# Kernel tuning notes

Hardware: AMD Instinct MI355X
Metric: run time of the kernel (lower is better)

Reference implementation:

```python
import jax, jax.numpy as jnp
from jax import lax
import numpy as np

SHAPE = (50, 60, 65)   # -> after net: (17, 27, 32), flatten = 14688
NEG = 0.01             # LeakyReLU default slope
B, N = 8, 80000        # batch size, total active voxels


def _lrelu(x):
    return jnp.where(x >= 0, x, NEG * x)


def _sparse_conv(x, w, b, m):
    # Regular (non-submanifold) sparse conv == dense VALID conv on densified
    # input (inactive sites are 0 so they contribute nothing). Output site is
    # active iff any input site in the kernel footprint is active; bias is
    # added only at active output sites.
    k = w.shape[2]
    y = lax.conv_general_dilated(x, w, (1, 1, 1), 'VALID',
                                 dimension_numbers=('NCDHW', 'OIDHW', 'NCDHW'))
    m2 = lax.reduce_window(m, 0.0, lax.max, (1, 1, k, k, k), (1, 1, 1, 1, 1), 'VALID')
    y = jnp.where(m2 > 0, y + b[None, :, None, None, None], 0.0)
    return y, m2


def _sparse_maxpool(x, m, k):
    # spconv SparseMaxPool: max over ACTIVE sites only (inactive excluded, not 0)
    xm = jnp.where(m > 0, x, -jnp.inf)
    p = lax.reduce_window(xm, -jnp.inf, lax.max, (1, 1, k, k, k), (1, 1, 1, 1, 1), 'VALID')
    m2 = lax.reduce_window(m, 0.0, lax.max, (1, 1, k, k, k), (1, 1, 1, 1, 1), 'VALID')
    return jnp.where(m2 > 0, p, 0.0), m2


def setup_inputs() -> dict:
    key = jax.random.key(0)
    ks = jax.random.split(key, 24)
    D, H, W = SHAPE
    features = jax.random.normal(ks[0], (N, 1), dtype=jnp.float32)
    bi = jax.random.randint(ks[1], (N,), 0, B)
    zi = jax.random.randint(ks[2], (N,), 0, D)
    yi = jax.random.randint(ks[3], (N,), 0, H)
    xi = jax.random.randint(ks[4], (N,), 0, W)
    coors = jnp.stack([bi, zi, yi, xi], axis=1).astype(jnp.int32)
    s = 0.05
    p = {}
    p['w1'] = jax.random.normal(ks[5], (32, 1, 4, 4, 4), jnp.float32) * s
    p['b1'] = jax.random.normal(ks[6], (32,), jnp.float32) * s
    p['w2'] = jax.random.normal(ks[7], (32, 32, 4, 4, 4), jnp.float32) * s
    p['b2'] = jax.random.normal(ks[8], (32,), jnp.float32) * s
    p['w3'] = jax.random.normal(ks[9], (32, 32, 4, 4, 4), jnp.float32) * s
    p['b3'] = jax.random.normal(ks[10], (32,), jnp.float32) * s
    p['w4'] = jax.random.normal(ks[11], (32, 32, 4, 4, 4), jnp.float32) * s
    p['b4'] = jax.random.normal(ks[12], (32,), jnp.float32) * s
    p['w5'] = jax.random.normal(ks[13], (32, 32, 4, 4, 4), jnp.float32) * s
    p['b5'] = jax.random.normal(ks[14], (32,), jnp.float32) * s
    p['w6'] = jax.random.normal(ks[15], (32, 32, 4, 4, 4), jnp.float32) * s
    p['b6'] = jax.random.normal(ks[16], (32,), jnp.float32) * s
    p['w7'] = jax.random.normal(ks[17], (1, 32, 4, 4, 4), jnp.float32) * s
    p['b7'] = jax.random.normal(ks[18], (1,), jnp.float32) * s
    p['W8'] = jax.random.normal(ks[19], (14688, 1000), jnp.float32) * 0.01
    p['b8'] = jax.random.normal(ks[20], (1000,), jnp.float32) * s
    p['W9'] = jax.random.normal(ks[21], (1000, 1000), jnp.float32) * 0.03
    p['b9'] = jax.random.normal(ks[22], (1000,), jnp.float32) * s
    p['W10'] = jax.random.normal(ks[23], (1000, 1), jnp.float32) * 0.03
    p['b10'] = jnp.zeros((1,), jnp.float32)
    return dict(features=features, coors=coors, batch_size=B, **p)


def reference(features, coors, batch_size,
              w1, b1, w2, b2, w3, b3, w4, b4, w5, b5, w6, b6, w7, b7,
              W8, b8, W9, b9, W10, b10):
    D, H, W = SHAPE
    bi, zi, yi, xi = coors[:, 0], coors[:, 1], coors[:, 2], coors[:, 3]
    dense = jnp.zeros((batch_size, 1, D, H, W), features.dtype)
    dense = dense.at[bi, 0, zi, yi, xi].set(features[:, 0])
    mask = jnp.zeros((batch_size, 1, D, H, W), features.dtype)
    mask = mask.at[bi, 0, zi, yi, xi].set(1.0)

    x, m = _sparse_conv(dense, w1, b1, mask); x = _lrelu(x)
    x, m = _sparse_conv(x, w2, b2, m);        x = _lrelu(x)
    x, m = _sparse_maxpool(x, m, 5)
    x, m = _sparse_conv(x, w3, b3, m);        x = _lrelu(x)
    x, m = _sparse_conv(x, w4, b4, m);        x = _lrelu(x)
    x, m = _sparse_maxpool(x, m, 5)
    x, m = _sparse_conv(x, w5, b5, m);        x = _lrelu(x)
    x, m = _sparse_conv(x, w6, b6, m);        x = _lrelu(x)
    x, m = _sparse_conv(x, w7, b7, m);        x = _lrelu(x)
    x, m = _sparse_maxpool(x, m, 5)

    # ToDense (inactive sites already 0) + Flatten -> [B, 14688]
    h = x.reshape(x.shape[0], -1)
    h = _lrelu(h @ W8 + b8)
    h = _lrelu(h @ W9 + b9)
    out = _lrelu(h @ W10 + b10)
    return out
```

## Files before the change

### kernel.cpp

```cpp
#include <hip/hip_runtime.h>
#include <cstddef>


#define NEGSLOPE 0.01f
#define NINF (-3.0e38f)

#define TZ 4
#define TY 4
#define TXT 16
#define IZ 7
#define IY 7
#define IX 19
#define NV (IZ*IY*IX)

#define PCZ 10

typedef __attribute__((ext_vector_type(8)))  short    short8;
typedef __attribute__((ext_vector_type(4)))  unsigned uint4v;
typedef __attribute__((ext_vector_type(16))) float    floatx16;

constexpr int ilog2c(int v) { return v == 1 ? 0 : 1 + ilog2c(v / 2); }

__device__ __forceinline__ float lrelu(float v) { return v >= 0.f ? v : NEGSLOPE * v; }

__device__ __forceinline__ unsigned short f2bf(float f) {
  unsigned b = __float_as_uint(f);
  return (unsigned short)((b + 0x7fffu + ((b >> 16) & 1u)) >> 16);
}
__device__ __forceinline__ float bf2f(unsigned short h) {
  return __uint_as_float(((unsigned)h) << 16);
}
__device__ __forceinline__ unsigned splitpair(float a, float b, unsigned& lo) {
  unsigned short ha = f2bf(a), hb = f2bf(b);
  unsigned short la = f2bf(a - bf2f(ha)), lb = f2bf(b - bf2f(hb));
  lo = (unsigned)la | ((unsigned)lb << 16);
  return (unsigned)ha | ((unsigned)hb << 16);
}

__device__ __forceinline__ float4 max4(float4 a, float4 b) {
  float4 r;
  r.x = fmaxf(a.x, b.x); r.y = fmaxf(a.y, b.y);
  r.z = fmaxf(a.z, b.z); r.w = fmaxf(a.w, b.w);
  return r;
}

__device__ __forceinline__ short8 ld_frag(const uint2* s2, int v, int oct) {
  uint2 u0 = s2[v * 5 + oct * 2];
  uint2 u1 = s2[v * 5 + oct * 2 + 1];
  uint4v t; t.x = u0.x; t.y = u0.y; t.z = u1.x; t.w = u1.y;
  return __builtin_bit_cast(short8, t);
}

__global__ void k_claim(const int* __restrict__ coors, unsigned* __restrict__ claim, int N) {
  int i = blockIdx.x * blockDim.x + threadIdx.x;
  if (i >= N) return;
  int b = coors[4*i], z = coors[4*i+1], y = coors[4*i+2], x = coors[4*i+3];
  int v = ((b*50 + z)*60 + y)*65 + x;
  atomicMax(&claim[v], (unsigned)(i + 1));
}

__global__ void k_scatter(const int* __restrict__ coors, const float* __restrict__ feat,
                          const unsigned* __restrict__ claim,
                          float* __restrict__ x0, float* __restrict__ m0, int N) {
  int i = blockIdx.x * blockDim.x + threadIdx.x;
  if (i >= N) return;
  int b = coors[4*i], z = coors[4*i+1], y = coors[4*i+2], x = coors[4*i+3];
  int v = ((b*50 + z)*60 + y)*65 + x;
  m0[v] = 1.f;
  if (claim[v] == (unsigned)(i + 1)) x0[v] = feat[i];
}

__global__ void k_repack(const float* __restrict__ w, float* __restrict__ wr, int CI, int CO) {
  int i = blockIdx.x * blockDim.x + threadIdx.x;
  int tot = CO * CI * 64;
  if (i >= tot) return;
  int k = i & 63;
  int ci = (i >> 6) % CI;
  int co = i / (64 * CI);
  wr[(k * CI + ci) * CO + co] = w[i];
}

__global__ void k_repack_mfma5(const float* __restrict__ wA, const float* __restrict__ wB,
                               const float* __restrict__ wC, const float* __restrict__ wD,
                               const float* __restrict__ wE, unsigned short* __restrict__ tbl0) {
  int layer = blockIdx.y;
  const float* w = layer == 0 ? wA : layer == 1 ? wB : layer == 2 ? wC
                 : layer == 3 ? wD : wE;
  unsigned short* tbl = tbl0 + (size_t)layer * 262144;
  int i = blockIdx.x * blockDim.x + threadIdx.x;
  if (i >= 64*4*2*64) return;
  int lane = i & 63; int t = i >> 6;
  int pack = t & 1; t >>= 1;
  int pass = t & 3; int tap = t >> 2;
  int co = lane & 31; int oct = lane >> 5;
#pragma unroll
  for (int j = 0; j < 8; ++j) {
    int k = oct * 8 + j;
    int ci = pass * 8 + (k & 7);
    int part = ((k >> 3) ^ pack) & 1;
    float wv = w[((co * 32 + ci) << 6) + tap];
    unsigned short wh = f2bf(wv);
    unsigned short r = part ? f2bf(wv - bf2f(wh)) : wh;
    tbl[(size_t)i * 8 + j] = r;
  }
}

template<int K>
__global__ __launch_bounds__(256, 4)
void kd_fused(const float* __restrict__ in, float* __restrict__ out,
              int Zi, int Yi, int Xi, int Zo, int Yo, int Xo,
              int tilesZ, int tilesY, int tilesX) {
  constexpr int TDZ = 4, TDY = 8, TDX = 32;
  constexpr int HZ = TDZ + K - 1, HY = TDY + K - 1, HX = TDX + K - 1;
  __shared__ float sA[HZ * HY * HX];
  __shared__ float sB[TDZ * HY * HX];
  __shared__ float sC[TDZ * TDY * HX];
  int bid = blockIdx.x;
  int txi = bid % tilesX; bid /= tilesX;
  int tyi = bid % tilesY; bid /= tilesY;
  int tzi = bid % tilesZ; int item = bid / tilesZ;
  const int z0 = tzi * TDZ, y0 = tyi * TDY, x0 = txi * TDX;
  const int tid = threadIdx.x;
  const float* ib = in + (size_t)item * Zi * Yi * Xi;

  for (int idx = tid; idx < HZ * HY * HX; idx += 256) {
    int iz = idx / (HY * HX); int r = idx - iz * (HY * HX);
    int iy = r / HX; int ix = r - iy * HX;
    int gz = z0 + iz, gy = y0 + iy, gx = x0 + ix;
    float v = 0.f;
    if (gz < Zi && gy < Yi && gx < Xi) v = ib[((size_t)gz * Yi + gy) * Xi + gx];
    sA[idx] = v;
  }
  __syncthreads();
  for (int idx = tid; idx < TDZ * HY * HX; idx += 256) {
    int z = idx / (HY * HX); int r = idx - z * (HY * HX);
    float m = 0.f;
#pragma unroll
    for (int d = 0; d < K; ++d) m = fmaxf(m, sA[(z + d) * (HY * HX) + r]);
    sB[idx] = m;
  }
  __syncthreads();
  for (int idx = tid; idx < TDZ * TDY * HX; idx += 256) {
    int z = idx / (TDY * HX); int r = idx - z * (TDY * HX);
    int y = r / HX; int x = r - y * HX;
    float m = 0.f;
#pragma unroll
    for (int d = 0; d < K; ++d) m = fmaxf(m, sB[z * (HY * HX) + (y + d) * HX + x]);
    sC[idx] = m;
  }
  __syncthreads();
  const int perOut = Zo * Yo * Xo;
  for (int idx = tid; idx < TDZ * TDY * TDX; idx += 256) {
    int z = idx / (TDY * TDX); int r = idx - z * (TDY * TDX);
    int y = r / TDX; int x = r - y * TDX;
    int gz = z0 + z, gy = y0 + y, gx = x0 + x;
    if (gz < Zo && gy < Yo && gx < Xo) {
      float m = 0.f;
#pragma unroll
      for (int d = 0; d < K; ++d) m = fmaxf(m, sC[z * (TDY * HX) + y * HX + x + d]);
      out[(size_t)item * perOut + ((size_t)gz * Yo + gy) * Xo + gx] = m;
    }
  }
}

template<int TZL, int TYL, int TXL, int IZL, int IYL, int IXL, bool POOLOUT>
__global__ __launch_bounds__(256, 4)
void k_conv32m(const float* __restrict__ in, const unsigned short* __restrict__ tbl,
               const float* __restrict__ bias, const float* __restrict__ mo,
               float* __restrict__ out,
               int Zi, int Yi, int Xi, int Zo, int Yo, int Xo,
               int tilesZ, int tilesY, int tilesX) {
  constexpr int NVL = IZL * IYL * IXL;
  constexpr int LXs = ilog2c(TXL);
  constexpr int LYs = ilog2c(TYL);
  __shared__ unsigned sU[NVL * 10];
  const int perIn = Zi * Yi * Xi;
  const int perOut = Zo * Yo * Xo;
  int bid = blockIdx.x;
  int txi = bid % tilesX; bid /= tilesX;
  int tyi = bid % tilesY; bid /= tilesY;
  int tzi = bid % tilesZ; int item = bid / tilesZ;
  const int z0 = tzi * TZL, y0 = tyi * TYL, x0 = txi * TXL;
  const int tid = threadIdx.x;
  const int lane = tid & 63;
  const int col = lane & 31;
  const int oct = lane >> 5;
  const int wv  = tid >> 6;

  int lvBase0, lvBase1;
  {
    int vt0 = (2*wv + 0)*32 + col;
    int vt1 = (2*wv + 1)*32 + col;
    lvBase0 = ((vt0 >> (LXs+LYs))*IYL + ((vt0 >> LXs) & (TYL-1)))*IXL + (vt0 & (TXL-1));
    lvBase1 = ((vt1 >> (LXs+LYs))*IYL + ((vt1 >> LXs) & (TYL-1)))*IXL + (vt1 & (TXL-1));
  }

  floatx16 acc0, acc1;
#pragma unroll
  for (int r = 0; r < 16; ++r) { acc0[r] = 0.f; acc1[r] = 0.f; }

  const float* inb = in + (size_t)item * perIn * 32;
  const char* tb = (const char*)tbl + lane * 16;
  uint2* s2 = (uint2*)sU;

#pragma unroll 1
  for (int p = 0; p < 4; ++p) {
    __syncthreads();
    for (int idx = tid; idx < NVL; idx += 256) {
      int iz = idx / (IYL * IXL); int r = idx - iz * (IYL * IXL);
      int iy = r / IXL; int ix = r - iy * IXL;
      int gz = z0 + iz, gy = y0 + iy, gx = x0 + ix;
      float4 f0 = make_float4(0.f,0.f,0.f,0.f), f1 = make_float4(0.f,0.f,0.f,0.f);
      if (gz < Zi && gy < Yi && gx < Xi) {
        const float* vp = inb + (size_t)((gz * Yi + gy) * Xi + gx) * 32 + p * 8;
        f0 = *(const float4*)vp;
        f1 = *(const float4*)(vp + 4);
      }
      unsigned l0, l1, l2, l3;
      unsigned h0 = splitpair(f0.x, f0.y, l0);
      unsigned h1 = splitpair(f0.z, f0.w, l1);
      unsigned h2 = splitpair(f1.x, f1.y, l2);
      unsigned h3 = splitpair(f1.z, f1.w, l3);
      s2[idx * 5 + 0] = make_uint2(h0, h1);
      s2[idx * 5 + 1] = make_uint2(h2, h3);
      s2[idx * 5 + 2] = make_uint2(l0, l1);
      s2[idx * 5 + 3] = make_uint2(l2, l3);
    }
    __syncthreads();

    const char* tp = tb + (size_t)p * 2048;
#pragma unroll 2
    for (int tap = 0; tap < 64; ++tap) {
      int kz = tap >> 4, ky = (tap >> 2) & 3, kx = tap & 3;
      int sOff = (kz * IYL + ky) * IXL + kx;
      short8 b0 = *(const short8*)(tp + (size_t)tap * 8192);
      short8 b1 = *(const short8*)(tp + (size_t)tap * 8192 + 1024);
      short8 a0 = ld_frag(s2, lvBase0 + sOff, oct);
      short8 a1 = ld_frag(s2, lvBase1 + sOff, oct);
      acc0 = __builtin_amdgcn_mfma_f32_32x32x16_bf16(a0, b0, acc0, 0, 0, 0);
      acc0 = __builtin_amdgcn_mfma_f32_32x32x16_bf16(a0, b1, acc0, 0, 0, 0);
      acc1 = __builtin_amdgcn_mfma_f32_32x32x16_bf16(a1, b0, acc1, 0, 0, 0);
      acc1 = __builtin_amdgcn_mfma_f32_32x32x16_bf16(a1, b1, acc1, 0, 0, 0);
    }
  }

  const float bco = bias[col];
#pragma unroll
  for (int gg = 0; gg < 2; ++gg) {
    int vtb = (2*wv + gg) * 32;
#pragma unroll
    for (int rg = 0; rg < 16; ++rg) {
      int row = (rg & 3) + 8 * (rg >> 2) + 4 * oct;
      int vt = vtb + row;
      int oz = vt >> (LXs+LYs), oy = (vt >> LXs) & (TYL-1), ox = vt & (TXL-1);
      int gz = z0 + oz, gy = y0 + oy, gx = x0 + ox;
      if (gz < Zo && gy < Yo && gx < Xo) {
        int ov = item * perOut + (gz * Yo + gy) * Xo + gx;
        float val = (gg == 0) ? acc0[rg] : acc1[rg];
        bool act = mo[ov] > 0.f;
        float vv = act ? lrelu(val + bco) : (POOLOUT ? NINF : 0.f);
        out[(size_t)ov * 32 + col] = vv;
      }
    }
  }
}

template<int TZL, int TYL, int TXL, int IZL, int IYL, int IXL, bool POOLOUT>
static void launch_conv32(hipStream_t stream,
                          const float* in, const unsigned short* tbl, const float* bias,
                          const float* mo, float* o,
                          int Zi, int Yi, int Xi, int Zo, int Yo, int Xo, int nI) {
  int tz = (Zo + TZL - 1) / TZL, ty = (Yo + TYL - 1) / TYL, tx = (Xo + TXL - 1) / TXL;
  k_conv32m<TZL,TYL,TXL,IZL,IYL,IXL,POOLOUT><<<nI * tz * ty * tx, 256, 0, stream>>>(
      in, tbl, bias, mo, o, Zi, Yi, Xi, Zo, Yo, Xo, tz, ty, tx);
}

__global__ __launch_bounds__(256, 2)
void k_conv1t(const float* __restrict__ in, const float* __restrict__ wr,
              const float* __restrict__ bias, const float* __restrict__ mo,
              float* __restrict__ out,
              int Zi, int Yi, int Xi, int Zo, int Yo, int Xo,
              int tilesZ, int tilesY, int tilesX) {
  __shared__ float sinf[NV];
  __shared__ float4 wsh[512];
  {
    const float4* wr4 = (const float4*)wr;
    for (int idx = threadIdx.x; idx < 512; idx += 256) wsh[idx] = wr4[idx];
  }
  const int perIn = Zi * Yi * Xi;
  const int perOut = Zo * Yo * Xo;
  int bid = blockIdx.x;
  int txi = bid % tilesX; bid /= tilesX;
  int tyi = bid % tilesY; bid /= tilesY;
  int tzi = bid % tilesZ; int item = bid / tilesZ;
  const int z0 = tzi * TZ, y0 = tyi * TY, x0 = txi * TXT;
  const int tid = threadIdx.x;
  const int ox = tid & 15, oy = (tid >> 4) & 3, oz = tid >> 6;

  const float* inb = in + (size_t)item * perIn;
  for (int idx = tid; idx < NV; idx += 256) {
    int iz = idx / (IY * IX); int r = idx - iz * (IY * IX);
    int iy = r / IX; int ix = r - iy * IX;
    int gz = z0 + iz, gy = y0 + iy, gx = x0 + ix;
    float val = 0.f;
    if (gz < Zi && gy < Yi && gx < Xi)
      val = inb[(size_t)((gz * Yi + gy) * Xi + gx)];
    sinf[idx] = val;
  }
  __syncthreads();

  float4 acc[8];
#pragma unroll
  for (int j = 0; j < 8; ++j) acc[j] = make_float4(0.f, 0.f, 0.f, 0.f);

#pragma unroll 1
  for (int tap = 0; tap < 64; ++tap) {
    int kz = tap >> 4, ky = (tap >> 2) & 3, kx = tap & 3;
    int lv = ((oz + kz) * IY + (oy + ky)) * IX + (ox + kx);
    float av = sinf[lv];
#pragma unroll
    for (int j = 0; j < 8; ++j) {
      float4 wvv = wsh[tap * 8 + j];
      acc[j].x = fmaf(av, wvv.x, acc[j].x);
      acc[j].y = fmaf(av, wvv.y, acc[j].y);
      acc[j].z = fmaf(av, wvv.z, acc[j].z);
      acc[j].w = fmaf(av, wvv.w, acc[j].w);
    }
  }

  int gz = z0 + oz, gy = y0 + oy, gx = x0 + ox;
  if (gz < Zo && gy < Yo && gx < Xo) {
    int ov = item * perOut + (gz * Yo + gy) * Xo + gx;
    bool act = mo[ov] > 0.f;
    const float4* b4 = (const float4*)bias;
    float* op = out + (size_t)ov * 32;
#pragma unroll
    for (int j = 0; j < 8; ++j) {
      float4 r = acc[j]; float4 bj = b4[j];
      r.x = lrelu(act ? (r.x + bj.x) : 0.f);
      r.y = lrelu(act ? (r.y + bj.y) : 0.f);
      r.z = lrelu(act ? (r.z + bj.z) : 0.f);
      r.w = lrelu(act ? (r.w + bj.w) : 0.f);
      *(float4*)(op + j * 4) = r;
    }
  }
}

__global__ __launch_bounds__(256, 2)
void k_conv7t(const float* __restrict__ in, const float* __restrict__ wr,
              const float* __restrict__ bias, const float* __restrict__ mo,
              float* __restrict__ out,
              int Zi, int Yi, int Xi, int Zo, int Yo, int Xo,
              int tilesZ, int tilesY, int tilesX) {
  __shared__ float4 sin4[4][NV];
  __shared__ float4 wsh[512];
  {
    const float4* wr4 = (const float4*)wr;
    for (int idx = threadIdx.x; idx < 512; idx += 256) wsh[idx] = wr4[idx];
  }
  const int perIn = Zi * Yi * Xi;
  const int perOut = Zo * Yo * Xo;
  int bid = blockIdx.x;
  int txi = bid % tilesX; bid /= tilesX;
  int tyi = bid % tilesY; bid /= tilesY;
  int tzi = bid % tilesZ; int item = bid / tilesZ;
  const int z0 = tzi * TZ, y0 = tyi * TY, x0 = txi * TXT;
  const int tid = threadIdx.x;
  const int ox = tid & 15, oy = (tid >> 4) & 3, oz = tid >> 6;

  const float* inb = in + (size_t)item * perIn * 32;
  float acc = 0.f;

#pragma unroll 1
  for (int h = 0; h < 2; ++h) {
    __syncthreads();
    for (int idx = tid; idx < NV * 4; idx += 256) {
      int q = idx / NV; int v = idx - q * NV;
      int iz = v / (IY * IX); int r = v - iz * (IY * IX);
      int iy = r / IX; int ix = r - iy * IX;
      int gz = z0 + iz, gy = y0 + iy, gx = x0 + ix;
      float4 val = make_float4(0.f, 0.f, 0.f, 0.f);
      if (gz < Zi && gy < Yi && gx < Xi)
        val = *(const float4*)(inb + (size_t)((gz * Yi + gy) * Xi + gx) * 32 + h * 16 + q * 4);
      sin4[q][v] = val;
    }
    __syncthreads();
#pragma unroll 1
    for (int tap = 0; tap < 64; ++tap) {
      int kz = tap >> 4, ky = (tap >> 2) & 3, kx = tap & 3;
      int lv = ((oz + kz) * IY + (oy + ky)) * IX + (ox + kx);
      float4 a0 = sin4[0][lv];
      float4 a1 = sin4[1][lv];
      float4 a2 = sin4[2][lv];
      float4 a3 = sin4[3][lv];
      float4 w0 = wsh[tap * 8 + h * 4 + 0];
      float4 w1 = wsh[tap * 8 + h * 4 + 1];
      float4 w2 = wsh[tap * 8 + h * 4 + 2];
      float4 w3 = wsh[tap * 8 + h * 4 + 3];
      acc += a0.x*w0.x + a0.y*w0.y + a0.z*w0.z + a0.w*w0.w
           + a1.x*w1.x + a1.y*w1.y + a1.z*w1.z + a1.w*w1.w
           + a2.x*w2.x + a2.y*w2.y + a2.z*w2.z + a2.w*w2.w
           + a3.x*w3.x + a3.y*w3.y + a3.z*w3.z + a3.w*w3.w;
    }
  }

  int gz = z0 + oz, gy = y0 + oy, gx = x0 + ox;
  if (gz < Zo && gy < Yo && gx < Xo) {
    int ov = item * perOut + (gz * Yo + gy) * Xo + gx;
    bool act = mo[ov] > 0.f;
    out[ov] = act ? lrelu(acc + bias[0]) : NINF;
  }
}

__global__ void k_pool_zw(const float* __restrict__ in, float* __restrict__ out,
                          int Zi, int Yi, int Xi, int Zo, int nI) {
  int gid = blockIdx.x * blockDim.x + threadIdx.x;
  int nCh = (Zo + PCZ - 1) / PCZ;
  int perI = nCh * Yi * Xi * 8;
  if (gid >= nI * perI) return;
  int c4 = gid & 7; int t = gid >> 3;
  int x = t % Xi; t /= Xi;
  int y = t % Yi; t /= Yi;
  int ch = t % nCh; int item = t / nCh;
  int z0 = ch * PCZ;
  int zend = z0 + PCZ; if (zend > Zo) zend = Zo;

  const float* colp = in + ((size_t)((item * Zi) * Yi + y) * Xi + x) * 32 + c4 * 4;
  const size_t zs = (size_t)Yi * Xi * 32;
  float* ocolp = out + ((size_t)((item * Zo) * Yi + y) * Xi + x) * 32 + c4 * 4;

  float4 w0 = *(const float4*)(colp + (size_t)(z0 + 0) * zs);
  float4 w1 = *(const float4*)(colp + (size_t)(z0 + 1) * zs);
  float4 w2 = *(const float4*)(colp + (size_t)(z0 + 2) * zs);
  float4 w3 = *(const float4*)(colp + (size_t)(z0 + 3) * zs);
#pragma unroll 2
  for (int z = z0; z < zend; ++z) {
    float4 c = *(const float4*)(colp + (size_t)(z + 4) * zs);
    float4 m = max4(max4(w0, w1), max4(w2, max4(w3, c)));
    *(float4*)(ocolp + (size_t)z * zs) = m;
    w0 = w1; w1 = w2; w2 = w3; w3 = c;
  }
}

__global__ void k_pool_yx(const float* __restrict__ in, const float* __restrict__ mp,
                          float* __restrict__ out,
                          int Z, int Yi, int Xi, int Yo, int Xo, int nI) {
  int gid = blockIdx.x * blockDim.x + threadIdx.x;
  int runsX = (Xo + 3) >> 2;
  int perR = Z * Yo * runsX;
  int tot = nI * perR * 8;
  if (gid >= tot) return;
  int c4 = gid & 7; int r = gid >> 3;
  int item = r / perR;
  int rr = r - item * perR;
  int xr = rr % runsX; int t = rr / runsX;
  int y = t % Yo; int z = t / Yo;
  int x0 = xr << 2;
  const float* ib = in + (size_t)item * Z * Yi * Xi * 32;

  float4 ym[8];
#pragma unroll
  for (int dx = 0; dx < 8; ++dx) ym[dx] = make_float4(NINF, NINF, NINF, NINF);
#pragma unroll
  for (int dy = 0; dy < 5; ++dy) {
    const float* rowb = ib + (size_t)((z * Yi + y + dy) * Xi) * 32;
#pragma unroll
    for (int dx = 0; dx < 8; ++dx) {
      int xx = x0 + dx;
      if (xx < Xi) {
        float4 v = *(const float4*)(rowb + (size_t)xx * 32 + c4 * 4);
        ym[dx] = max4(ym[dx], v);
      }
    }
  }
  int perOut = Z * Yo * Xo;
#pragma unroll
  for (int j = 0; j < 4; ++j) {
    int xx = x0 + j;
    if (xx < Xo) {
      float4 a = ym[j];
#pragma unroll
      for (int d = 1; d < 5; ++d) a = max4(a, ym[j + d]);
      int v = item * perOut + (z * Yo + y) * Xo + xx;
      bool act = mp[v] > 0.f;
      float4 rrv;
      rrv.x = act ? a.x : 0.f; rrv.y = act ? a.y : 0.f;
      rrv.z = act ? a.z : 0.f; rrv.w = act ? a.w : 0.f;
      *(float4*)(out + (size_t)v*32 + c4*4) = rrv;
    }
  }
}

__global__ void k_pool3(const float* __restrict__ xin,
                        const float* __restrict__ mp, float* __restrict__ out, int nI) {
  int gid = blockIdx.x * blockDim.x + threadIdx.x;
  int perOut = 17 * 27 * 32;
  int tot = nI * perOut;
  if (gid >= tot) return;
  int item = gid / perOut;
  int r = gid - item * perOut;
  int x = r & 31; int t = r >> 5;
  int y = t % 27; int z = t / 27;
  const float* xb = xin + (size_t)item * 23436;
  float acc = NINF;
  for (int dz = 0; dz < 5; dz++)
    for (int dy = 0; dy < 5; dy++) {
      const float* rowx = xb + (size_t)(((z + dz)*31 + y + dy)*36 + x);
      for (int dx = 0; dx < 5; dx++)
        acc = fmaxf(acc, rowx[dx]);
    }
  out[gid] = (mp[gid] > 0.f) ? acc : 0.f;
}

__global__ __launch_bounds__(256, 4)
void k_fc_part(const float* __restrict__ X, const float* __restrict__ Wm,
               float* __restrict__ part, int K, int Ncol, int Kc) {
  __shared__ float sm[16][16][8];
  int ks = blockIdx.y;
  int k0 = ks * Kc;
  int k1 = k0 + Kc; if (k1 > K) k1 = K;
  int cl = threadIdx.x & 15;
  int kt = threadIdx.x >> 4;
  int col = blockIdx.x * 16 + cl;
  float a0=0.f,a1=0.f,a2=0.f,a3=0.f,a4=0.f,a5=0.f,a6=0.f,a7=0.f;
  if (col < Ncol) {
    for (int k = k0 + kt; k < k1; k += 16) {
      float w = Wm[(size_t)k * Ncol + col];
      a0 += X[0 * K + k] * w; a1 += X[1 * K + k] * w;
      a2 += X[2 * K + k] * w; a3 += X[3 * K + k] * w;
      a4 += X[4 * K + k] * w; a5 += X[5 * K + k] * w;
      a6 += X[6 * K + k] * w; a7 += X[7 * K + k] * w;
    }
  }
  sm[kt][cl][0]=a0; sm[kt][cl][1]=a1; sm[kt][cl][2]=a2; sm[kt][cl][3]=a3;
  sm[kt][cl][4]=a4; sm[kt][cl][5]=a5; sm[kt][cl][6]=a6; sm[kt][cl][7]=a7;
  __syncthreads();
  if (threadIdx.x < 128) {
    int c = threadIdx.x & 15;
    int b = threadIdx.x >> 4;
    float s = 0.f;
#pragma unroll
    for (int k = 0; k < 16; k++) s += sm[k][c][b];
    int cc = blockIdx.x * 16 + c;
    if (cc < Ncol) part[((size_t)ks * 8 + b) * Ncol + cc] = s;
  }
}

__global__ void k_fc_fin(const float* __restrict__ part, int ns,
                         const float* __restrict__ bias, float* __restrict__ out, int Ncol) {
  int i = blockIdx.x * blockDim.x + threadIdx.x;
  if (i >= 8 * Ncol) return;
  int b = i / Ncol;
  int c = i - b * Ncol;
  float s = 0.f;
  for (int ks = 0; ks < ns; ks++) s += part[((size_t)ks * 8 + b) * Ncol + c];
  out[i] = lrelu(s + bias[c]);
}

__global__ __launch_bounds__(256, 4)
void k_fc(const float* __restrict__ X, const float* __restrict__ Wm,
          const float* __restrict__ bias, float* __restrict__ out,
          int K, int Ncol) {
  __shared__ float sm[16][16][8];
  int cl = threadIdx.x & 15;
  int kt = threadIdx.x >> 4;
  int col = blockIdx.x * 16 + cl;
  float a0=0.f,a1=0.f,a2=0.f,a3=0.f,a4=0.f,a5=0.f,a6=0.f,a7=0.f;
  if (col < Ncol) {
    for (int k = kt; k < K; k += 16) {
      float w = Wm[(size_t)k * Ncol + col];
      a0 += X[0 * K + k] * w; a1 += X[1 * K + k] * w;
      a2 += X[2 * K + k] * w; a3 += X[3 * K + k] * w;
      a4 += X[4 * K + k] * w; a5 += X[5 * K + k] * w;
      a6 += X[6 * K + k] * w; a7 += X[7 * K + k] * w;
    }
  }
  sm[kt][cl][0]=a0; sm[kt][cl][1]=a1; sm[kt][cl][2]=a2; sm[kt][cl][3]=a3;
  sm[kt][cl][4]=a4; sm[kt][cl][5]=a5; sm[kt][cl][6]=a6; sm[kt][cl][7]=a7;
  __syncthreads();
  if (threadIdx.x < 128) {
    int c = threadIdx.x & 15;
    int b = threadIdx.x >> 4;
    float s = 0.f;
#pragma unroll
    for (int k = 0; k < 16; k++) s += sm[k][c][b];
    int cc = blockIdx.x * 16 + c;
    if (cc < Ncol) out[b * Ncol + cc] = lrelu(s + bias[cc]);
  }
}

static inline int G256(long long n) { return (int)((n + 255) / 256); }

extern "C" void kernel_launch(void* const* d_in, const int* in_sizes, int n_in,
                              void* d_out, int out_size, void* d_ws, size_t ws_size,
                              hipStream_t stream) {
  const float* feat  = (const float*)d_in[0];
  const int*   coors = (const int*)d_in[1];
  const float* w1 = (const float*)d_in[3];  const float* b1 = (const float*)d_in[4];
  const float* w2 = (const float*)d_in[5];  const float* b2 = (const float*)d_in[6];
  const float* w3 = (const float*)d_in[7];  const float* b3 = (const float*)d_in[8];
  const float* w4 = (const float*)d_in[9];  const float* b4 = (const float*)d_in[10];
  const float* w5 = (const float*)d_in[11]; const float* b5 = (const float*)d_in[12];
  const float* w6 = (const float*)d_in[13]; const float* b6 = (const float*)d_in[14];
  const float* w7 = (const float*)d_in[15]; const float* b7 = (const float*)d_in[16];
  const float* W8 = (const float*)d_in[17]; const float* b8 = (const float*)d_in[18];
  const float* W9 = (const float*)d_in[19]; const float* b9 = (const float*)d_in[20];
  const float* W10= (const float*)d_in[21]; const float* b10= (const float*)d_in[22];
  float* out = (float*)d_out;

  char* ws = (char*)d_ws;
  size_t off = 0;
  auto alloc = [&](size_t nfloats) -> float* {
    float* p = (float*)(ws + off);
    off += ((nfloats * 4 + 1023) / 1024) * 1024;
    return p;
  };

  float* x0  = alloc(1560000);
  float* m0  = alloc(1560000);
  float* m1  = alloc(8 * 166098);
  float* m2  = alloc(8 * 140184);
  float* mp1 = alloc(8 * 110000);
  float* m3  = alloc(8 * 90428);
  float* m4  = alloc(8 * 73304);
  float* mp2 = alloc(8 * 54000);
  float* m5  = alloc(8 * 41958);
  float* m6  = alloc(8 * 31824);
  float* m7  = alloc(8 * 23436);
  float* mp3 = alloc(8 * 14688);
  float* p3  = alloc(8 * 14688);
  float* wr1 = alloc(2048);
  float* wr7 = alloc(2048);
  unsigned short* tb2 = (unsigned short*)alloc(131072);
  unsigned short* tb3 = (unsigned short*)alloc(131072);
  unsigned short* tb4 = (unsigned short*)alloc(131072);
  unsigned short* tb5 = (unsigned short*)alloc(131072);
  unsigned short* tb6 = (unsigned short*)alloc(131072);
  float* part= alloc(64000);
  float* h8  = alloc(8000);
  float* h9  = alloc(8000);
  size_t fixedOff = off;

  const size_t perItemAB = ((size_t)5315136*4 + 1023)/1024*1024
                         + ((size_t)4485888*4 + 1023)/1024*1024
                         + ((size_t)23436*4 + 1023)/1024*1024;
  int G = 0;
  for (int g : {8, 4, 2, 1})
    if (fixedOff + (size_t)g * perItemAB <= ws_size) { G = g; break; }
  if (G == 0) return;

  float* A  = alloc((size_t)G * 5315136);
  float* Bb = alloc((size_t)G * 4485888);
  float* x7 = alloc((size_t)G * 23436);
  unsigned* claim = (unsigned*)A;

  hipMemsetAsync(claim, 0, 1560000 * 4, stream);
  hipMemsetAsync(x0,    0, 1560000 * 4, stream);
  hipMemsetAsync(m0,    0, 1560000 * 4, stream);

  k_repack<<<G256(32*1*64),  256, 0, stream>>>(w1, wr1, 1, 32);
  k_repack<<<G256(1*32*64),  256, 0, stream>>>(w7, wr7, 32, 1);
  k_repack_mfma5<<<dim3(128, 5), 256, 0, stream>>>(w2, w3, w4, w5, w6, tb2);

  const int N = 80000;
  k_claim  <<<G256(N), 256, 0, stream>>>(coors, claim, N);
  k_scatter<<<G256(N), 256, 0, stream>>>(coors, feat, claim, x0, m0, N);

  auto dil3 = [&](const float* src, float* dst,
                  int Zi, int Yi, int Xi, int Zo, int Yo, int Xo, int K) {
    int tz = (Zo + 3) / 4, ty = (Yo + 7) / 8, tx = (Xo + 31) / 32;
    if (K == 4)
      kd_fused<4><<<8 * tz * ty * tx, 256, 0, stream>>>(src, dst, Zi,Yi,Xi, Zo,Yo,Xo, tz,ty,tx);
    else
      kd_fused<5><<<8 * tz * ty * tx, 256, 0, stream>>>(src, dst, Zi,Yi,Xi, Zo,Yo,Xo, tz,ty,tx);
  };
  dil3(m0,  m1,  50,60,65, 47,57,62, 4);
  dil3(m1,  m2,  47,57,62, 44,54,59, 4);
  dil3(m2,  mp1, 44,54,59, 40,50,55, 5);
  dil3(mp1, m3,  40,50,55, 37,47,52, 4);
  dil3(m3,  m4,  37,47,52, 34,44,49, 4);
  dil3(m4,  mp2, 34,44,49, 30,40,45, 5);
  dil3(mp2, m5,  30,40,45, 27,37,42, 4);
  dil3(m5,  m6,  27,37,42, 24,34,39, 4);
  dil3(m6,  m7,  24,34,39, 21,31,36, 4);
  dil3(m7,  mp3, 21,31,36, 17,27,32, 5);

  for (int g0 = 0; g0 < 8; g0 += G) {
    const float* x0g  = x0  + (size_t)g0 * 195000;
    const float* m1g  = m1  + (size_t)g0 * 166098;
    const float* m2g  = m2  + (size_t)g0 * 140184;
    const float* mp1g = mp1 + (size_t)g0 * 110000;
    const float* m3g  = m3  + (size_t)g0 * 90428;
    const float* m4g  = m4  + (size_t)g0 * 73304;
    const float* mp2g = mp2 + (size_t)g0 * 54000;
    const float* m5g  = m5  + (size_t)g0 * 41958;
    const float* m6g  = m6  + (size_t)g0 * 31824;
    const float* m7g  = m7  + (size_t)g0 * 23436;
    const float* mp3g = mp3 + (size_t)g0 * 14688;

    {
      int tz = (47 + TZ - 1) / TZ, ty = (57 + TY - 1) / TY, tx = (62 + TXT - 1) / TXT;
      k_conv1t<<<G * tz * ty * tx, 256, 0, stream>>>(
          x0g, wr1, b1, m1g, A, 50,60,65, 47,57,62, tz, ty, tx);
    }
    launch_conv32<4,4,16,7,7,19,true>(stream, A, tb2, b2, m2g, Bb, 47,57,62, 44,54,59, G);
    {
      int nCh = (40 + PCZ - 1) / PCZ;
      k_pool_zw<<<G256((long long)G * nCh * 54 * 59 * 8), 256, 0, stream>>>(Bb, A, 44,54,59, 40, G);
    }
    k_pool_yx<<<G256((long long)G*40*50*14*8), 256, 0, stream>>>(A, mp1g, Bb, 40,54,59, 50,55, G);
    launch_conv32<8,8,4,11,11,7,false>(stream, Bb, tb3, b3, m3g, A, 40,50,55, 37,47,52, G);
    launch_conv32<4,16,4,7,19,7,true>(stream, A, tb4, b4, m4g, Bb, 37,47,52, 34,44,49, G);
    {
      int nCh = (30 + PCZ - 1) / PCZ;
      k_pool_zw<<<G256((long long)G * nCh * 44 * 49 * 8), 256, 0, stream>>>(Bb, A, 34,44,49, 30, G);
    }
    k_pool_yx<<<G256((long long)G*30*40*12*8), 256, 0, stream>>>(A, mp2g, Bb, 30,44,49, 40,45, G);
    launch_conv32<4,4,16,7,7,19,false>(stream, Bb, tb5, b5, m5g, A, 30,40,45, 27,37,42, G);
    launch_conv32<8,4,8,11,7,11,false>(stream, A, tb6, b6, m6g, Bb, 27,37,42, 24,34,39, G);
    {
      int tz = (21 + TZ - 1) / TZ, ty = (31 + TY - 1) / TY, tx = (36 + TXT - 1) / TXT;
      k_conv7t<<<G * tz * ty * tx, 256, 0, stream>>>(
          Bb, wr7, b7, m7g, x7, 24,34,39, 21,31,36, tz, ty, tx);
    }
    k_pool3<<<G256((long long)G*14688), 256, 0, stream>>>(
        x7, mp3g, p3 + (size_t)g0 * 14688, G);
  }

  k_fc_part<<<dim3(63, 8), 256, 0, stream>>>(p3, W8, part, 14688, 1000, 1836);
  k_fc_fin <<<G256(8000), 256, 0, stream>>>(part, 8, b8, h8, 1000);
  k_fc_part<<<dim3(63, 4), 256, 0, stream>>>(h8, W9, part, 1000, 1000, 250);
  k_fc_fin <<<G256(8000), 256, 0, stream>>>(part, 4, b9, h9, 1000);
  k_fc<<<1, 256, 0, stream>>>(h9, W10, b10, out, 1000, 1);
}
```

Baseline: 2.991 ms.

## Fuse mask dilation pairs, merge repack kernels and memsets, raise conv1t occupancy

Mask dilation now runs as five kernels, each computing two successive max-dilations from one shared-memory halo tile and writing both outputs, instead of ten separate kernels. This cuts launches and the global reread of the intermediate mask, at the cost of larger shared memory (launch bounds lowered to 2 blocks) and redundant halo recomputation. The three weight repack kernels become one launch, and the two memsets become one call that assumes x0 and m0 are contiguous. k_conv1t launch bounds are raised to 4 waves per SIMD.

```diff
diff --git a/kernel.cpp b/kernel.cpp
--- a/kernel.cpp
+++ b/kernel.cpp
@@ -70,24 +70,25 @@
   if (claim[v] == (unsigned)(i + 1)) x0[v] = feat[i];
 }
 
-__global__ void k_repack(const float* __restrict__ w, float* __restrict__ wr, int CI, int CO) {
+__global__ void k_repack_all(const float* __restrict__ wA, const float* __restrict__ wB,
+                             const float* __restrict__ wC, const float* __restrict__ wD,
+                             const float* __restrict__ wE,
+                             const float* __restrict__ w1, const float* __restrict__ w7,
+                             unsigned short* __restrict__ tbl0,
+                             float* __restrict__ wr1, float* __restrict__ wr7) {
+  int layer = blockIdx.y;
   int i = blockIdx.x * blockDim.x + threadIdx.x;
-  int tot = CO * CI * 64;
-  if (i >= tot) return;
-  int k = i & 63;
-  int ci = (i >> 6) % CI;
-  int co = i / (64 * CI);
-  wr[(k * CI + ci) * CO + co] = w[i];
-}
-
-__global__ void k_repack_mfma5(const float* __restrict__ wA, const float* __restrict__ wB,
-                               const float* __restrict__ wC, const float* __restrict__ wD,
-                               const float* __restrict__ wE, unsigned short* __restrict__ tbl0) {
-  int layer = blockIdx.y;
+  if (layer >= 5) {
+    if (i < 2048) {
+      int k = i & 63;
+      if (layer == 5) { int co = i >> 6; wr1[k * 32 + co] = w1[i]; }
+      else           { int ci = (i >> 6) & 31; wr7[k * 32 + ci] = w7[i]; }
+    }
+    return;
+  }
   const float* w = layer == 0 ? wA : layer == 1 ? wB : layer == 2 ? wC
                  : layer == 3 ? wD : wE;
   unsigned short* tbl = tbl0 + (size_t)layer * 262144;
-  int i = blockIdx.x * blockDim.x + threadIdx.x;
   if (i >= 64*4*2*64) return;
   int lane = i & 63; int t = i >> 6;
   int pack = t & 1; t >>= 1;
@@ -105,60 +106,90 @@
   }
 }
 
-template<int K>
-__global__ __launch_bounds__(256, 4)
-void kd_fused(const float* __restrict__ in, float* __restrict__ out,
-              int Zi, int Yi, int Xi, int Zo, int Yo, int Xo,
-              int tilesZ, int tilesY, int tilesX) {
+template<int K1, int K2>
+__global__ __launch_bounds__(256, 2)
+void kd_fused2(const float* __restrict__ in, float* __restrict__ out1,
+               float* __restrict__ out2,
+               int Z0, int Y0, int X0, int Z1, int Y1, int X1,
+               int Z2, int Y2, int X2,
+               int tilesZ, int tilesY, int tilesX) {
   constexpr int TDZ = 4, TDY = 8, TDX = 32;
-  constexpr int HZ = TDZ + K - 1, HY = TDY + K - 1, HX = TDX + K - 1;
-  __shared__ float sA[HZ * HY * HX];
-  __shared__ float sB[TDZ * HY * HX];
-  __shared__ float sC[TDZ * TDY * HX];
+  constexpr int H1Z = TDZ + K2 - 1, H1Y = TDY + K2 - 1, H1X = TDX + K2 - 1;
+  constexpr int H0Z = H1Z + K1 - 1, H0Y = H1Y + K1 - 1, H0X = H1X + K1 - 1;
+  __shared__ float sA[H0Z * H0Y * H0X];
+  __shared__ float sB[H1Z * H0Y * H0X];
   int bid = blockIdx.x;
   int txi = bid % tilesX; bid /= tilesX;
   int tyi = bid % tilesY; bid /= tilesY;
   int tzi = bid % tilesZ; int item = bid / tilesZ;
   const int z0 = tzi * TDZ, y0 = tyi * TDY, x0 = txi * TDX;
   const int tid = threadIdx.x;
-  const float* ib = in + (size_t)item * Zi * Yi * Xi;
-
-  for (int idx = tid; idx < HZ * HY * HX; idx += 256) {
-    int iz = idx / (HY * HX); int r = idx - iz * (HY * HX);
-    int iy = r / HX; int ix = r - iy * HX;
+  const float* ib = in + (size_t)item * Z0 * Y0 * X0;
+
+  for (int idx = tid; idx < H0Z * H0Y * H0X; idx += 256) {
+    int iz = idx / (H0Y * H0X); int r = idx - iz * (H0Y * H0X);
+    int iy = r / H0X; int ix = r - iy * H0X;
     int gz = z0 + iz, gy = y0 + iy, gx = x0 + ix;
     float v = 0.f;
-    if (gz < Zi && gy < Yi && gx < Xi) v = ib[((size_t)gz * Yi + gy) * Xi + gx];
+    if (gz < Z0 && gy < Y0 && gx < X0) v = ib[((size_t)gz * Y0 + gy) * X0 + gx];
     sA[idx] = v;
   }
   __syncthreads();
-  for (int idx = tid; idx < TDZ * HY * HX; idx += 256) {
-    int z = idx / (HY * HX); int r = idx - z * (HY * HX);
+  for (int idx = tid; idx < H1Z * H0Y * H0X; idx += 256) {
+    int z = idx / (H0Y * H0X); int r = idx - z * (H0Y * H0X);
     float m = 0.f;
 #pragma unroll
-    for (int d = 0; d < K; ++d) m = fmaxf(m, sA[(z + d) * (HY * HX) + r]);
+    for (int d = 0; d < K1; ++d) m = fmaxf(m, sA[(z + d) * (H0Y * H0X) + r]);
     sB[idx] = m;
   }
   __syncthreads();
-  for (int idx = tid; idx < TDZ * TDY * HX; idx += 256) {
-    int z = idx / (TDY * HX); int r = idx - z * (TDY * HX);
-    int y = r / HX; int x = r - y * HX;
+  for (int idx = tid; idx < H1Z * H1Y * H0X; idx += 256) {
+    int z = idx / (H1Y * H0X); int r = idx - z * (H1Y * H0X);
+    int y = r / H0X; int x = r - y * H0X;
     float m = 0.f;
 #pragma unroll
-    for (int d = 0; d < K; ++d) m = fmaxf(m, sB[z * (HY * HX) + (y + d) * HX + x]);
-    sC[idx] = m;
-  }
-  __syncthreads();
-  const int perOut = Zo * Yo * Xo;
+    for (int d = 0; d < K1; ++d) m = fmaxf(m, sB[z * (H0Y * H0X) + (y + d) * H0X + x]);
+    sA[idx] = m;
+  }
+  __syncthreads();
+  for (int idx = tid; idx < H1Z * H1Y * H1X; idx += 256) {
+    int z = idx / (H1Y * H1X); int r = idx - z * (H1Y * H1X);
+    int y = r / H1X; int x = r - y * H1X;
+    float m = 0.f;
+#pragma unroll
+    for (int d = 0; d < K1; ++d) m = fmaxf(m, sA[z * (H1Y * H0X) + y * H0X + x + d]);
+    sB[idx] = m;
+    int gz = z0 + z, gy = y0 + y, gx = x0 + x;
+    if (gz < Z1 && gy < Y1 && gx < X1)
+      out1[(size_t)item * Z1 * Y1 * X1 + ((size_t)gz * Y1 + gy) * X1 + gx] = m;
+  }
+  __syncthreads();
+  for (int idx = tid; idx < TDZ * H1Y * H1X; idx += 256) {
+    int z = idx / (H1Y * H1X); int r = idx - z * (H1Y * H1X);
+    float m = 0.f;
+#pragma unroll
+    for (int d = 0; d < K2; ++d) m = fmaxf(m, sB[(z + d) * (H1Y * H1X) + r]);
+    sA[idx] = m;
+  }
+  __syncthreads();
+  for (int idx = tid; idx < TDZ * TDY * H1X; idx += 256) {
+    int z = idx / (TDY * H1X); int r = idx - z * (TDY * H1X);
+    int y = r / H1X; int x = r - y * H1X;
+    float m = 0.f;
+#pragma unroll
+    for (int d = 0; d < K2; ++d) m = fmaxf(m, sA[z * (H1Y * H1X) + (y + d) * H1X + x]);
+    sB[idx] = m;
+  }
+  __syncthreads();
   for (int idx = tid; idx < TDZ * TDY * TDX; idx += 256) {
     int z = idx / (TDY * TDX); int r = idx - z * (TDY * TDX);
     int y = r / TDX; int x = r - y * TDX;
     int gz = z0 + z, gy = y0 + y, gx = x0 + x;
-    if (gz < Zo && gy < Yo && gx < Xo) {
+    if (gz < Z2 && gy < Y2 && gx < X2) {
       float m = 0.f;
 #pragma unroll
-      for (int d = 0; d < K; ++d) m = fmaxf(m, sC[z * (TDY * HX) + y * HX + x + d]);
-      out[(size_t)item * perOut + ((size_t)gz * Yo + gy) * Xo + gx] = m;
+      for (int d = 0; d < K2; ++d) m = fmaxf(m, sB[z * (TDY * H1X) + y * H1X + x + d]);
+      out2[(size_t)item * Z2 * Y2 * X2 + ((size_t)gz * Y2 + gy) * X2 + gx] = m;
     }
   }
 }
@@ -275,7 +306,7 @@
       in, tbl, bias, mo, o, Zi, Yi, Xi, Zo, Yo, Xo, tz, ty, tx);
 }
 
-__global__ __launch_bounds__(256, 2)
+__global__ __launch_bounds__(256, 4)
 void k_conv1t(const float* __restrict__ in, const float* __restrict__ wr,
               const float* __restrict__ bias, const float* __restrict__ mo,
               float* __restrict__ out,
@@ -655,35 +686,32 @@
   unsigned* claim = (unsigned*)A;
 
   hipMemsetAsync(claim, 0, 1560000 * 4, stream);
-  hipMemsetAsync(x0,    0, 1560000 * 4, stream);
-  hipMemsetAsync(m0,    0, 1560000 * 4, stream);
-
-  k_repack<<<G256(32*1*64),  256, 0, stream>>>(w1, wr1, 1, 32);
-  k_repack<<<G256(1*32*64),  256, 0, stream>>>(w7, wr7, 32, 1);
-  k_repack_mfma5<<<dim3(128, 5), 256, 0, stream>>>(w2, w3, w4, w5, w6, tb2);
+  hipMemsetAsync(x0, 0, 6240256 + 6240000, stream);
+
+  k_repack_all<<<dim3(128, 7), 256, 0, stream>>>(w2, w3, w4, w5, w6, w1, w7,
+                                                 tb2, wr1, wr7);
 
   const int N = 80000;
   k_claim  <<<G256(N), 256, 0, stream>>>(coors, claim, N);
   k_scatter<<<G256(N), 256, 0, stream>>>(coors, feat, claim, x0, m0, N);
 
-  auto dil3 = [&](const float* src, float* dst,
-                  int Zi, int Yi, int Xi, int Zo, int Yo, int Xo, int K) {
-    int tz = (Zo + 3) / 4, ty = (Yo + 7) / 8, tx = (Xo + 31) / 32;
-    if (K == 4)
-      kd_fused<4><<<8 * tz * ty * tx, 256, 0, stream>>>(src, dst, Zi,Yi,Xi, Zo,Yo,Xo, tz,ty,tx);
+  auto dil2 = [&](const float* src, float* o1, float* o2,
+                  int Z0,int Y0,int X0, int Z1,int Y1,int X1, int Z2,int Y2,int X2,
+                  int K1, int K2) {
+    int tz = (Z2 + 3) / 4, ty = (Y2 + 7) / 8, tx = (X2 + 31) / 32;
+    int g = 8 * tz * ty * tx;
+    if (K1 == 4 && K2 == 4)
+      kd_fused2<4,4><<<g, 256, 0, stream>>>(src, o1, o2, Z0,Y0,X0, Z1,Y1,X1, Z2,Y2,X2, tz,ty,tx);
+    else if (K1 == 5)
+      kd_fused2<5,4><<<g, 256, 0, stream>>>(src, o1, o2, Z0,Y0,X0, Z1,Y1,X1, Z2,Y2,X2, tz,ty,tx);
     else
-      kd_fused<5><<<8 * tz * ty * tx, 256, 0, stream>>>(src, dst, Zi,Yi,Xi, Zo,Yo,Xo, tz,ty,tx);
+      kd_fused2<4,5><<<g, 256, 0, stream>>>(src, o1, o2, Z0,Y0,X0, Z1,Y1,X1, Z2,Y2,X2, tz,ty,tx);
   };
-  dil3(m0,  m1,  50,60,65, 47,57,62, 4);
-  dil3(m1,  m2,  47,57,62, 44,54,59, 4);
-  dil3(m2,  mp1, 44,54,59, 40,50,55, 5);
-  dil3(mp1, m3,  40,50,55, 37,47,52, 4);
-  dil3(m3,  m4,  37,47,52, 34,44,49, 4);
-  dil3(m4,  mp2, 34,44,49, 30,40,45, 5);
-  dil3(mp2, m5,  30,40,45, 27,37,42, 4);
-  dil3(m5,  m6,  27,37,42, 24,34,39, 4);
-  dil3(m6,  m7,  24,34,39, 21,31,36, 4);
-  dil3(m7,  mp3, 21,31,36, 17,27,32, 5);
+  dil2(m0,  m1, m2,  50,60,65, 47,57,62, 44,54,59, 4,4);
+  dil2(m2,  mp1, m3, 44,54,59, 40,50,55, 37,47,52, 5,4);
+  dil2(m3,  m4, mp2, 37,47,52, 34,44,49, 30,40,45, 4,5);
+  dil2(mp2, m5, m6,  30,40,45, 27,37,42, 24,34,39, 4,4);
+  dil2(m6,  m7, mp3, 24,34,39, 21,31,36, 17,27,32, 4,5);
 
   for (int g0 = 0; g0 < 8; g0 += G) {
     const float* x0g  = x0  + (size_t)g0 * 195000;
```

After: 3.074 ms. 1.03x slower.
